# Performance work log

Hardware: AMD Instinct MI355X
Metric: run time of the kernel (lower is better)

Reference implementation:

```python
import jax, jax.numpy as jnp
import numpy as np

B, N, H, F_IN, F_OUT = 16, 512, 8, 128, 128
NEG_SLOPE = 0.2


def setup_inputs() -> dict:
    key = jax.random.key(0)
    k_h, k_adj, k_bias, k_W, k_a = jax.random.split(key, 5)
    h = jax.random.normal(k_h, (B, N, F_IN), dtype=jnp.float32)
    # Binary adjacency (shared across batch); force self-loops so every row
    # of the masked softmax has at least one valid entry (avoids NaN rows).
    adj = jax.random.randint(k_adj, (N, N), 0, 2, dtype=jnp.int32)
    adj = adj.at[jnp.arange(N), jnp.arange(N)].set(1)
    bias_matrix = jax.random.normal(k_bias, (1, 1, N, N), dtype=jnp.float32)
    # Xavier-uniform-like init for params
    lim_W = float(np.sqrt(6.0 / (F_IN + F_OUT)))
    W = jax.random.uniform(k_W, (H, F_IN, F_OUT), minval=-lim_W, maxval=lim_W, dtype=jnp.float32)
    lim_a = float(np.sqrt(6.0 / (2 * F_OUT + 1)))
    a = jax.random.uniform(k_a, (H, 2 * F_OUT, 1), minval=-lim_a, maxval=lim_a, dtype=jnp.float32)
    return {"h": h, "adj": adj, "bias_matrix": bias_matrix, "W": W, "a": a}


def reference(h, adj, bias_matrix, W, a):
    # h: [B,N,Fin], adj: [N,N] int, bias_matrix: [1,1,N,N], W: [H,Fin,F], a: [H,2F,1]
    f = W.shape[-1]
    h_prime = jnp.einsum('bni,hio->bnho', h, W)  # [B,N,H,F]
    # e[b,i,j,h] = leakyrelu(a_h . concat(h_prime[b,i,h], h_prime[b,j,h]))
    # Decompose a into src/dst halves: identical math, avoids O(B*N*N*H*2F) cat.
    a_src = a[:, :f, 0]  # [H,F]
    a_dst = a[:, f:, 0]  # [H,F]
    s_src = jnp.einsum('bnhf,hf->bnh', h_prime, a_src)  # score contribution of node i
    s_dst = jnp.einsum('bnhf,hf->bnh', h_prime, a_dst)  # score contribution of node j
    e = jax.nn.leaky_relu(s_src[:, :, None, :] + s_dst[:, None, :, :], NEG_SLOPE)  # [B,N,N,H]
    e = e + bias_matrix[0, 0][None, :, :, None]  # bias broadcast over batch & heads
    mask = (adj != 0)[None, :, :, None]  # [1,N,N,1] -> broadcast [B,N,N,H]
    e = jnp.where(mask, e, -jnp.inf)
    attention = jax.nn.softmax(e, axis=2)  # softmax over neighbors j
    h_out = jnp.einsum('bijh,bjhf->bihf', attention, h_prime)  # [B,N,H,F]
    # concat=False -> mean over heads
    return h_out.mean(axis=2)  # [B,N,F]
```

## Files before the change

### kernel.cpp

```cpp
#include <hip/hip_runtime.h>
#include <hip/hip_bf16.h>

#define NB 16
#define NN 512
#define NH 8
#define NF 128
#define NEG_SLOPE 0.2f

typedef short bf16x8 __attribute__((ext_vector_type(8)));
typedef unsigned short u16x8 __attribute__((ext_vector_type(8)));
typedef float f32x4 __attribute__((ext_vector_type(4)));

__device__ inline unsigned short f2bf(float x) {
    __hip_bfloat16 b = __float2bfloat16(x);
    return __builtin_bit_cast(unsigned short, b);
}
__device__ inline float bf2f(unsigned short u) {
    return __uint_as_float(((unsigned int)u) << 16);
}

__global__ __launch_bounds__(256) void prep_all_kernel(
    const float* __restrict__ h, const int* __restrict__ adj,
    const float* __restrict__ bias, const float* __restrict__ W,
    const float* __restrict__ a,
    float* __restrict__ mb,
    unsigned short* __restrict__ hHi, unsigned short* __restrict__ hLo,
    unsigned short* __restrict__ wtHi, unsigned short* __restrict__ wtLo,
    float* __restrict__ wasrc, float* __restrict__ wadst)
{
    int t = blockIdx.x * 256 + threadIdx.x;
    {
        float v = h[t];
        unsigned short hi = f2bf(v);
        hHi[t] = hi;
        hLo[t] = f2bf(v - bf2f(hi));
    }
    if (t < NN * NN) mb[t] = (adj[t] != 0) ? bias[t] : -1.0e30f;
    if (t < NH * NF * NF) {
        float v = W[t];
        int hh = t >> 14;
        int k  = (t >> 7) & 127;
        int f  = t & 127;
        int u  = (hh * NF + f) * NF + k;
        unsigned short hi = f2bf(v);
        wtHi[u] = hi;
        wtLo[u] = f2bf(v - bf2f(hi));
    }
    if (t < NH * NF) {
        int hh = t >> 7, i = t & 127;
        const float* wrow = W + (hh * NF + i) * NF;
        const float* asr = a + hh * 2 * NF;
        const float* ads = asr + NF;
        float s1 = 0.f, s2 = 0.f;
        #pragma unroll 4
        for (int f = 0; f < NF; ++f) {
            float w = wrow[f];
            s1 = fmaf(w, asr[f], s1);
            s2 = fmaf(w, ads[f], s2);
        }
        wasrc[t] = s1; wadst[t] = s2;
    }
}

__global__ __launch_bounds__(256) void score_kernel(
    const float* __restrict__ h, const float* __restrict__ wasrc,
    const float* __restrict__ wadst, float* __restrict__ ssrc, float* __restrict__ sdstT)
{
    __shared__ float wsm[2][NH * (NF + 4)];
    int tid = threadIdx.x;
    for (int u = tid; u < NH * NF; u += 256) {
        int hh = u >> 7, f = u & 127;
        wsm[0][hh * (NF + 4) + f] = wasrc[u];
        wsm[1][hh * (NF + 4) + f] = wadst[u];
    }
    __syncthreads();
    int t = blockIdx.x * 256 + tid;
    int hh = t & 7;
    int bn = t >> 3;
    int b = bn >> 9, n = bn & 511;
    const float4* hrow = (const float4*)(h + (size_t)bn * NF);
    const float4* w1 = (const float4*)(&wsm[0][hh * (NF + 4)]);
    const float4* w2 = (const float4*)(&wsm[1][hh * (NF + 4)]);
    float s1 = 0.f, s2 = 0.f;
    #pragma unroll
    for (int u = 0; u < NF / 4; ++u) {
        float4 hv = hrow[u], a1 = w1[u], a2 = w2[u];
        s1 += hv.x * a1.x + hv.y * a1.y + hv.z * a1.z + hv.w * a1.w;
        s2 += hv.x * a2.x + hv.y * a2.y + hv.z * a2.z + hv.w * a2.w;
    }
    ssrc[t] = s1;
    sdstT[((size_t)(b * NH + hh)) * NN + n] = s2;
}

__global__ __launch_bounds__(256, 4) void hprime_kernel(
    const unsigned short* __restrict__ hHi, const unsigned short* __restrict__ hLo,
    const unsigned short* __restrict__ wtHi, const unsigned short* __restrict__ wtLo,
    unsigned short* __restrict__ hpT)
{
    int bx = blockIdx.x;
    int nchunk = bx & 63;
    int hfg = bx >> 6;
    int hh = hfg >> 1, fg = hfg & 1;
    int tid = threadIdx.x;
    int wave = tid >> 6, lane = tid & 63;
    int col = lane & 15, kg = lane >> 4;
    int fbase = hh * NF + fg * 64 + wave * 16;
    int n0g = nchunk * 128;
    int b = n0g >> 9;
    int nin = n0g & 511;

    const unsigned short* Bh = wtHi + (size_t)(fbase + col) * NF + kg * 8;
    const unsigned short* Bl = wtLo + (size_t)(fbase + col) * NF + kg * 8;
    bf16x8 bh[4], bl[4];
    #pragma unroll
    for (int ks = 0; ks < 4; ++ks) {
        bh[ks] = *(const bf16x8*)(Bh + ks * 32);
        bl[ks] = *(const bf16x8*)(Bl + ks * 32);
    }

    size_t outRow = ((size_t)b * (NH * NF) + fbase + col) * NN;

    #pragma unroll 2
    for (int nt = 0; nt < 8; ++nt) {
        const unsigned short* Ah = hHi + (size_t)(n0g + nt * 16 + col) * NF + kg * 8;
        const unsigned short* Al = hLo + (size_t)(n0g + nt * 16 + col) * NF + kg * 8;
        bf16x8 ah[4], al[4];
        #pragma unroll
        for (int ks = 0; ks < 4; ++ks) {
            ah[ks] = *(const bf16x8*)(Ah + ks * 32);
            al[ks] = *(const bf16x8*)(Al + ks * 32);
        }
        f32x4 acc = {0.f, 0.f, 0.f, 0.f};
        #pragma unroll
        for (int ks = 0; ks < 4; ++ks) {
            acc = __builtin_amdgcn_mfma_f32_16x16x32_bf16(ah[ks], bh[ks], acc, 0, 0, 0);
            acc = __builtin_amdgcn_mfma_f32_16x16x32_bf16(al[ks], bh[ks], acc, 0, 0, 0);
            acc = __builtin_amdgcn_mfma_f32_16x16x32_bf16(ah[ks], bl[ks], acc, 0, 0, 0);
        }
        ushort4 u;
        u.x = f2bf(acc[0]); u.y = f2bf(acc[1]);
        u.z = f2bf(acc[2]); u.w = f2bf(acc[3]);
        *(ushort4*)&hpT[outRow + nin + nt * 16 + kg * 4] = u;
    }
}

__global__ __launch_bounds__(512, 4) void attn_kernel(
    const unsigned short* __restrict__ hpT, const float* __restrict__ mb,
    const float* __restrict__ ssrc, const float* __restrict__ sdstT,
    float* __restrict__ out)
{
    __shared__ float red[NH][32][64];
    int bx = blockIdx.x;
    int b = bx & 15;
    int rest = bx >> 4;
    int ipair = rest >> 1;
    int fhalf = rest & 1;
    int i0 = ipair * 32;
    int f0 = fhalf * 64;
    int tid = threadIdx.x;
    int lane = tid & 63, h = tid >> 6;
    int col = lane & 15, kg = lane >> 4;

    const short one_bf = (short)0x3f80;
    const bf16x8 vone = {one_bf, one_bf, one_bf, one_bf, one_bf, one_bf, one_bf, one_bf};

    const float* sd = sdstT + (size_t)(b * NH + h) * NN;
    float s0 = ssrc[((size_t)(b * NN) + i0 + col) * NH + h];
    float s1 = ssrc[((size_t)(b * NN) + i0 + 16 + col) * NH + h];
    const float* mb0 = mb + (size_t)(i0 + col) * NN;
    const float* mb1 = mb + (size_t)(i0 + 16 + col) * NN;
    const unsigned short* Bbase = hpT + ((size_t)(b * NH + h) * NF + f0 + col) * NN;

    f32x4 acc[2][4];
    f32x4 accS[2];
    #pragma unroll
    for (int ti = 0; ti < 2; ++ti) {
        accS[ti] = (f32x4){0.f, 0.f, 0.f, 0.f};
        #pragma unroll
        for (int tf = 0; tf < 4; ++tf) acc[ti][tf] = (f32x4){0.f, 0.f, 0.f, 0.f};
    }

    for (int t = 0; t < 16; ++t) {
        int j0 = t * 32 + kg * 8;
        float4 sv0 = *(const float4*)(sd + j0);
        float4 sv1 = *(const float4*)(sd + j0 + 4);
        float4 m00 = *(const float4*)(mb0 + j0);
        float4 m01 = *(const float4*)(mb0 + j0 + 4);
        float4 m10 = *(const float4*)(mb1 + j0);
        float4 m11 = *(const float4*)(mb1 + j0 + 4);
        bf16x8 Bv0 = *(const bf16x8*)(Bbase + (size_t)0 * 16 * NN + j0);
        bf16x8 Bv1 = *(const bf16x8*)(Bbase + (size_t)1 * 16 * NN + j0);
        bf16x8 Bv2 = *(const bf16x8*)(Bbase + (size_t)2 * 16 * NN + j0);
        bf16x8 Bv3 = *(const bf16x8*)(Bbase + (size_t)3 * 16 * NN + j0);

        u16x8 a0, a1;
        {
            float x;
            x = s0 + sv0.x; x = x > 0.f ? x : NEG_SLOPE * x; a0[0] = f2bf(__expf(x + m00.x));
            x = s0 + sv0.y; x = x > 0.f ? x : NEG_SLOPE * x; a0[1] = f2bf(__expf(x + m00.y));
            x = s0 + sv0.z; x = x > 0.f ? x : NEG_SLOPE * x; a0[2] = f2bf(__expf(x + m00.z));
            x = s0 + sv0.w; x = x > 0.f ? x : NEG_SLOPE * x; a0[3] = f2bf(__expf(x + m00.w));
            x = s0 + sv1.x; x = x > 0.f ? x : NEG_SLOPE * x; a0[4] = f2bf(__expf(x + m01.x));
            x = s0 + sv1.y; x = x > 0.f ? x : NEG_SLOPE * x; a0[5] = f2bf(__expf(x + m01.y));
            x = s0 + sv1.z; x = x > 0.f ? x : NEG_SLOPE * x; a0[6] = f2bf(__expf(x + m01.z));
            x = s0 + sv1.w; x = x > 0.f ? x : NEG_SLOPE * x; a0[7] = f2bf(__expf(x + m01.w));
            x = s1 + sv0.x; x = x > 0.f ? x : NEG_SLOPE * x; a1[0] = f2bf(__expf(x + m10.x));
            x = s1 + sv0.y; x = x > 0.f ? x : NEG_SLOPE * x; a1[1] = f2bf(__expf(x + m10.y));
            x = s1 + sv0.z; x = x > 0.f ? x : NEG_SLOPE * x; a1[2] = f2bf(__expf(x + m10.z));
            x = s1 + sv0.w; x = x > 0.f ? x : NEG_SLOPE * x; a1[3] = f2bf(__expf(x + m10.w));
            x = s1 + sv1.x; x = x > 0.f ? x : NEG_SLOPE * x; a1[4] = f2bf(__expf(x + m11.x));
            x = s1 + sv1.y; x = x > 0.f ? x : NEG_SLOPE * x; a1[5] = f2bf(__expf(x + m11.y));
            x = s1 + sv1.z; x = x > 0.f ? x : NEG_SLOPE * x; a1[6] = f2bf(__expf(x + m11.z));
            x = s1 + sv1.w; x = x > 0.f ? x : NEG_SLOPE * x; a1[7] = f2bf(__expf(x + m11.w));
        }
        bf16x8 A0 = __builtin_bit_cast(bf16x8, a0);
        bf16x8 A1 = __builtin_bit_cast(bf16x8, a1);

        __builtin_amdgcn_s_setprio(1);
        acc[0][0] = __builtin_amdgcn_mfma_f32_16x16x32_bf16(A0, Bv0, acc[0][0], 0, 0, 0);
        acc[0][1] = __builtin_amdgcn_mfma_f32_16x16x32_bf16(A0, Bv1, acc[0][1], 0, 0, 0);
        acc[0][2] = __builtin_amdgcn_mfma_f32_16x16x32_bf16(A0, Bv2, acc[0][2], 0, 0, 0);
        acc[0][3] = __builtin_amdgcn_mfma_f32_16x16x32_bf16(A0, Bv3, acc[0][3], 0, 0, 0);
        accS[0]   = __builtin_amdgcn_mfma_f32_16x16x32_bf16(A0, vone, accS[0], 0, 0, 0);
        acc[1][0] = __builtin_amdgcn_mfma_f32_16x16x32_bf16(A1, Bv0, acc[1][0], 0, 0, 0);
        acc[1][1] = __builtin_amdgcn_mfma_f32_16x16x32_bf16(A1, Bv1, acc[1][1], 0, 0, 0);
        acc[1][2] = __builtin_amdgcn_mfma_f32_16x16x32_bf16(A1, Bv2, acc[1][2], 0, 0, 0);
        acc[1][3] = __builtin_amdgcn_mfma_f32_16x16x32_bf16(A1, Bv3, acc[1][3], 0, 0, 0);
        accS[1]   = __builtin_amdgcn_mfma_f32_16x16x32_bf16(A1, vone, accS[1], 0, 0, 0);
        __builtin_amdgcn_s_setprio(0);
    }

    #pragma unroll
    for (int ti = 0; ti < 2; ++ti)
        #pragma unroll
        for (int tf = 0; tf < 4; ++tf)
            #pragma unroll
            for (int r = 0; r < 4; ++r)
                red[h][ti * 16 + kg * 4 + r][tf * 16 + col] = acc[ti][tf][r] / accS[ti][r];
    __syncthreads();

    int i = tid >> 4;
    int fq = (tid & 15) * 4;
    float4 s = {0.f, 0.f, 0.f, 0.f};
    #pragma unroll
    for (int w = 0; w < NH; ++w) {
        float4 v = *(const float4*)&red[w][i][fq];
        s.x += v.x; s.y += v.y; s.z += v.z; s.w += v.w;
    }
    s.x *= 0.125f; s.y *= 0.125f; s.z *= 0.125f; s.w *= 0.125f;
    *(float4*)&out[((size_t)(b * NN) + i0 + i) * NF + f0 + fq] = s;
}

extern "C" void kernel_launch(void* const* d_in, const int* in_sizes, int n_in,
                              void* d_out, int out_size, void* d_ws, size_t ws_size,
                              hipStream_t stream)
{
    const float* h    = (const float*)d_in[0];
    const int*   adj  = (const int*)d_in[1];
    const float* bias = (const float*)d_in[2];
    const float* W    = (const float*)d_in[3];
    const float* a    = (const float*)d_in[4];
    float* out = (float*)d_out;

    char* ws = (char*)d_ws;
    unsigned short* hpT  = (unsigned short*)ws;   ws += (size_t)NB * NH * NF * NN * 2;
    float* mb    = (float*)ws;                    ws += (size_t)NN * NN * 4;
    float* ssrc  = (float*)ws;                    ws += (size_t)NB * NN * NH * 4;
    float* sdstT = (float*)ws;                    ws += (size_t)NB * NN * NH * 4;
    float* wasrc = (float*)ws;                    ws += NH * NF * 4;
    float* wadst = (float*)ws;                    ws += NH * NF * 4;
    unsigned short* hHi  = (unsigned short*)ws;   ws += (size_t)NB * NN * NF * 2;
    unsigned short* hLo  = (unsigned short*)ws;   ws += (size_t)NB * NN * NF * 2;
    unsigned short* wtHi = (unsigned short*)ws;   ws += (size_t)NH * NF * NF * 2;
    unsigned short* wtLo = (unsigned short*)ws;   ws += (size_t)NH * NF * NF * 2;

    hipLaunchKernelGGL(prep_all_kernel, dim3((NB * NN * NF) / 256), dim3(256), 0, stream,
                       h, adj, bias, W, a, mb, hHi, hLo, wtHi, wtLo, wasrc, wadst);
    hipLaunchKernelGGL(score_kernel, dim3((NB * NN * NH) / 256), dim3(256), 0, stream,
                       h, wasrc, wadst, ssrc, sdstT);
    hipLaunchKernelGGL(hprime_kernel, dim3(64 * 16), dim3(256), 0, stream,
                       hHi, hLo, wtHi, wtLo, hpT);
    hipLaunchKernelGGL(attn_kernel, dim3(NB * 32), dim3(512), 0, stream,
                       hpT, mb, ssrc, sdstT, out);
}
```

Baseline: 181.8 us.

## Precompute exp(bias) masked bf16 and widen attention tile to full feature width

The prep kernel now stores exp(bias) as bf16, with zero where there is no edge, in place of an fp32 additive mask. This halves mask traffic, and the exponent no longer has to absorb the bias. The attention kernel now covers all 128 features per block instead of 64. That halves the grid to 256 blocks and computes the softmax numerators once rather than twice per feature half. It also software-pipelines the score and mask loads, and does the head reduction in two passes to fit a smaller shared buffer. The trade-offs are more accumulator registers (launch bounds drop to 2 blocks per CU) and fewer blocks than the GPU has compute units.

```diff
diff --git a/kernel.cpp b/kernel.cpp
--- a/kernel.cpp
+++ b/kernel.cpp
@@ -23,7 +23,7 @@
     const float* __restrict__ h, const int* __restrict__ adj,
     const float* __restrict__ bias, const float* __restrict__ W,
     const float* __restrict__ a,
-    float* __restrict__ mb,
+    unsigned short* __restrict__ emb,
     unsigned short* __restrict__ hHi, unsigned short* __restrict__ hLo,
     unsigned short* __restrict__ wtHi, unsigned short* __restrict__ wtLo,
     float* __restrict__ wasrc, float* __restrict__ wadst)
@@ -35,7 +35,7 @@
         hHi[t] = hi;
         hLo[t] = f2bf(v - bf2f(hi));
     }
-    if (t < NN * NN) mb[t] = (adj[t] != 0) ? bias[t] : -1.0e30f;
+    if (t < NN * NN) emb[t] = (adj[t] != 0) ? f2bf(__expf(bias[t])) : (unsigned short)0;
     if (t < NH * NF * NF) {
         float v = W[t];
         int hh = t >> 14;
@@ -48,15 +48,15 @@
     }
     if (t < NH * NF) {
         int hh = t >> 7, i = t & 127;
-        const float* wrow = W + (hh * NF + i) * NF;
-        const float* asr = a + hh * 2 * NF;
-        const float* ads = asr + NF;
+        const float4* wrow = (const float4*)(W + (hh * NF + i) * NF);
+        const float4* asr = (const float4*)(a + hh * 2 * NF);
+        const float4* ads = (const float4*)(a + hh * 2 * NF + NF);
         float s1 = 0.f, s2 = 0.f;
-        #pragma unroll 4
-        for (int f = 0; f < NF; ++f) {
-            float w = wrow[f];
-            s1 = fmaf(w, asr[f], s1);
-            s2 = fmaf(w, ads[f], s2);
+        #pragma unroll 8
+        for (int f = 0; f < NF / 4; ++f) {
+            float4 w = wrow[f], x = asr[f], y = ads[f];
+            s1 += w.x * x.x + w.y * x.y + w.z * x.z + w.w * x.w;
+            s2 += w.x * y.x + w.y * y.y + w.z * y.z + w.w * y.w;
         }
         wasrc[t] = s1; wadst[t] = s2;
     }
@@ -144,19 +144,31 @@
     }
 }
 
-__global__ __launch_bounds__(512, 4) void attn_kernel(
-    const unsigned short* __restrict__ hpT, const float* __restrict__ mb,
+__device__ inline bf16x8 make_afrag(float s, float4 v0, float4 v1, bf16x8 eb) {
+    u16x8 ebu = __builtin_bit_cast(u16x8, eb);
+    u16x8 r;
+    float x;
+    x = s + v0.x; x = fmaxf(x, NEG_SLOPE * x); r[0] = f2bf(__expf(x) * bf2f(ebu[0]));
+    x = s + v0.y; x = fmaxf(x, NEG_SLOPE * x); r[1] = f2bf(__expf(x) * bf2f(ebu[1]));
+    x = s + v0.z; x = fmaxf(x, NEG_SLOPE * x); r[2] = f2bf(__expf(x) * bf2f(ebu[2]));
+    x = s + v0.w; x = fmaxf(x, NEG_SLOPE * x); r[3] = f2bf(__expf(x) * bf2f(ebu[3]));
+    x = s + v1.x; x = fmaxf(x, NEG_SLOPE * x); r[4] = f2bf(__expf(x) * bf2f(ebu[4]));
+    x = s + v1.y; x = fmaxf(x, NEG_SLOPE * x); r[5] = f2bf(__expf(x) * bf2f(ebu[5]));
+    x = s + v1.z; x = fmaxf(x, NEG_SLOPE * x); r[6] = f2bf(__expf(x) * bf2f(ebu[6]));
+    x = s + v1.w; x = fmaxf(x, NEG_SLOPE * x); r[7] = f2bf(__expf(x) * bf2f(ebu[7]));
+    return __builtin_bit_cast(bf16x8, r);
+}
+
+__global__ __launch_bounds__(512, 2) void attn_kernel(
+    const unsigned short* __restrict__ hpT, const unsigned short* __restrict__ emb,
     const float* __restrict__ ssrc, const float* __restrict__ sdstT,
     float* __restrict__ out)
 {
-    __shared__ float red[NH][32][64];
+    __shared__ float red[NH][16][NF + 4];
     int bx = blockIdx.x;
     int b = bx & 15;
-    int rest = bx >> 4;
-    int ipair = rest >> 1;
-    int fhalf = rest & 1;
+    int ipair = bx >> 4;
     int i0 = ipair * 32;
-    int f0 = fhalf * 64;
     int tid = threadIdx.x;
     int lane = tid & 63, h = tid >> 6;
     int col = lane & 15, kg = lane >> 4;
@@ -167,88 +179,79 @@
     const float* sd = sdstT + (size_t)(b * NH + h) * NN;
     float s0 = ssrc[((size_t)(b * NN) + i0 + col) * NH + h];
     float s1 = ssrc[((size_t)(b * NN) + i0 + 16 + col) * NH + h];
-    const float* mb0 = mb + (size_t)(i0 + col) * NN;
-    const float* mb1 = mb + (size_t)(i0 + 16 + col) * NN;
-    const unsigned short* Bbase = hpT + ((size_t)(b * NH + h) * NF + f0 + col) * NN;
-
-    f32x4 acc[2][4];
+    const unsigned short* eb0p = emb + (size_t)(i0 + col) * NN;
+    const unsigned short* eb1p = emb + (size_t)(i0 + 16 + col) * NN;
+    const unsigned short* Bbase = hpT + ((size_t)(b * NH + h) * NF + col) * NN;
+
+    f32x4 acc[2][8];
     f32x4 accS[2];
     #pragma unroll
     for (int ti = 0; ti < 2; ++ti) {
         accS[ti] = (f32x4){0.f, 0.f, 0.f, 0.f};
         #pragma unroll
-        for (int tf = 0; tf < 4; ++tf) acc[ti][tf] = (f32x4){0.f, 0.f, 0.f, 0.f};
-    }
-
+        for (int tf = 0; tf < 8; ++tf) acc[ti][tf] = (f32x4){0.f, 0.f, 0.f, 0.f};
+    }
+
+    float4 sv0[2], sv1[2];
+    bf16x8 eb0v[2], eb1v[2];
+    {
+        int j = kg * 8;
+        sv0[0] = *(const float4*)(sd + j);
+        sv1[0] = *(const float4*)(sd + j + 4);
+        eb0v[0] = *(const bf16x8*)(eb0p + j);
+        eb1v[0] = *(const bf16x8*)(eb1p + j);
+    }
+
+    #pragma unroll
     for (int t = 0; t < 16; ++t) {
-        int j0 = t * 32 + kg * 8;
-        float4 sv0 = *(const float4*)(sd + j0);
-        float4 sv1 = *(const float4*)(sd + j0 + 4);
-        float4 m00 = *(const float4*)(mb0 + j0);
-        float4 m01 = *(const float4*)(mb0 + j0 + 4);
-        float4 m10 = *(const float4*)(mb1 + j0);
-        float4 m11 = *(const float4*)(mb1 + j0 + 4);
-        bf16x8 Bv0 = *(const bf16x8*)(Bbase + (size_t)0 * 16 * NN + j0);
-        bf16x8 Bv1 = *(const bf16x8*)(Bbase + (size_t)1 * 16 * NN + j0);
-        bf16x8 Bv2 = *(const bf16x8*)(Bbase + (size_t)2 * 16 * NN + j0);
-        bf16x8 Bv3 = *(const bf16x8*)(Bbase + (size_t)3 * 16 * NN + j0);
-
-        u16x8 a0, a1;
-        {
-            float x;
-            x = s0 + sv0.x; x = x > 0.f ? x : NEG_SLOPE * x; a0[0] = f2bf(__expf(x + m00.x));
-            x = s0 + sv0.y; x = x > 0.f ? x : NEG_SLOPE * x; a0[1] = f2bf(__expf(x + m00.y));
-            x = s0 + sv0.z; x = x > 0.f ? x : NEG_SLOPE * x; a0[2] = f2bf(__expf(x + m00.z));
-            x = s0 + sv0.w; x = x > 0.f ? x : NEG_SLOPE * x; a0[3] = f2bf(__expf(x + m00.w));
-            x = s0 + sv1.x; x = x > 0.f ? x : NEG_SLOPE * x; a0[4] = f2bf(__expf(x + m01.x));
-            x = s0 + sv1.y; x = x > 0.f ? x : NEG_SLOPE * x; a0[5] = f2bf(__expf(x + m01.y));
-            x = s0 + sv1.z; x = x > 0.f ? x : NEG_SLOPE * x; a0[6] = f2bf(__expf(x + m01.z));
-            x = s0 + sv1.w; x = x > 0.f ? x : NEG_SLOPE * x; a0[7] = f2bf(__expf(x + m01.w));
-            x = s1 + sv0.x; x = x > 0.f ? x : NEG_SLOPE * x; a1[0] = f2bf(__expf(x + m10.x));
-            x = s1 + sv0.y; x = x > 0.f ? x : NEG_SLOPE * x; a1[1] = f2bf(__expf(x + m10.y));
-            x = s1 + sv0.z; x = x > 0.f ? x : NEG_SLOPE * x; a1[2] = f2bf(__expf(x + m10.z));
-            x = s1 + sv0.w; x = x > 0.f ? x : NEG_SLOPE * x; a1[3] = f2bf(__expf(x + m10.w));
-            x = s1 + sv1.x; x = x > 0.f ? x : NEG_SLOPE * x; a1[4] = f2bf(__expf(x + m11.x));
-            x = s1 + sv1.y; x = x > 0.f ? x : NEG_SLOPE * x; a1[5] = f2bf(__expf(x + m11.y));
-            x = s1 + sv1.z; x = x > 0.f ? x : NEG_SLOPE * x; a1[6] = f2bf(__expf(x + m11.z));
-            x = s1 + sv1.w; x = x > 0.f ? x : NEG_SLOPE * x; a1[7] = f2bf(__expf(x + m11.w));
-        }
-        bf16x8 A0 = __builtin_bit_cast(bf16x8, a0);
-        bf16x8 A1 = __builtin_bit_cast(bf16x8, a1);
+        const int cur = t & 1, nxt = cur ^ 1;
+        const int jc = t * 32 + kg * 8;
+        if (t < 15) {
+            const int jn = jc + 32;
+            sv0[nxt] = *(const float4*)(sd + jn);
+            sv1[nxt] = *(const float4*)(sd + jn + 4);
+            eb0v[nxt] = *(const bf16x8*)(eb0p + jn);
+            eb1v[nxt] = *(const bf16x8*)(eb1p + jn);
+        }
+        bf16x8 Bv[8];
+        #pragma unroll
+        for (int tf = 0; tf < 8; ++tf)
+            Bv[tf] = *(const bf16x8*)(Bbase + (size_t)tf * 16 * NN + jc);
+
+        bf16x8 A0 = make_afrag(s0, sv0[cur], sv1[cur], eb0v[cur]);
+        bf16x8 A1 = make_afrag(s1, sv0[cur], sv1[cur], eb1v[cur]);
 
         __builtin_amdgcn_s_setprio(1);
-        acc[0][0] = __builtin_amdgcn_mfma_f32_16x16x32_bf16(A0, Bv0, acc[0][0], 0, 0, 0);
-        acc[0][1] = __builtin_amdgcn_mfma_f32_16x16x32_bf16(A0, Bv1, acc[0][1], 0, 0, 0);
-        acc[0][2] = __builtin_amdgcn_mfma_f32_16x16x32_bf16(A0, Bv2, acc[0][2], 0, 0, 0);
-        acc[0][3] = __builtin_amdgcn_mfma_f32_16x16x32_bf16(A0, Bv3, acc[0][3], 0, 0, 0);
-        accS[0]   = __builtin_amdgcn_mfma_f32_16x16x32_bf16(A0, vone, accS[0], 0, 0, 0);
-        acc[1][0] = __builtin_amdgcn_mfma_f32_16x16x32_bf16(A1, Bv0, acc[1][0], 0, 0, 0);
-        acc[1][1] = __builtin_amdgcn_mfma_f32_16x16x32_bf16(A1, Bv1, acc[1][1], 0, 0, 0);
-        acc[1][2] = __builtin_amdgcn_mfma_f32_16x16x32_bf16(A1, Bv2, acc[1][2], 0, 0, 0);
-        acc[1][3] = __builtin_amdgcn_mfma_f32_16x16x32_bf16(A1, Bv3, acc[1][3], 0, 0, 0);
-        accS[1]   = __builtin_amdgcn_mfma_f32_16x16x32_bf16(A1, vone, accS[1], 0, 0, 0);
+        #pragma unroll
+        for (int tf = 0; tf < 8; ++tf) {
+            acc[0][tf] = __builtin_amdgcn_mfma_f32_16x16x32_bf16(A0, Bv[tf], acc[0][tf], 0, 0, 0);
+            acc[1][tf] = __builtin_amdgcn_mfma_f32_16x16x32_bf16(A1, Bv[tf], acc[1][tf], 0, 0, 0);
+        }
+        accS[0] = __builtin_amdgcn_mfma_f32_16x16x32_bf16(A0, vone, accS[0], 0, 0, 0);
+        accS[1] = __builtin_amdgcn_mfma_f32_16x16x32_bf16(A1, vone, accS[1], 0, 0, 0);
         __builtin_amdgcn_s_setprio(0);
     }
 
-    #pragma unroll
-    for (int ti = 0; ti < 2; ++ti)
-        #pragma unroll
-        for (int tf = 0; tf < 4; ++tf)
+    int fr = tid & 127;
+    int iq = tid >> 7;
+    #pragma unroll
+    for (int ti = 0; ti < 2; ++ti) {
+        #pragma unroll
+        for (int tf = 0; tf < 8; ++tf)
             #pragma unroll
             for (int r = 0; r < 4; ++r)
-                red[h][ti * 16 + kg * 4 + r][tf * 16 + col] = acc[ti][tf][r] / accS[ti][r];
-    __syncthreads();
-
-    int i = tid >> 4;
-    int fq = (tid & 15) * 4;
-    float4 s = {0.f, 0.f, 0.f, 0.f};
-    #pragma unroll
-    for (int w = 0; w < NH; ++w) {
-        float4 v = *(const float4*)&red[w][i][fq];
-        s.x += v.x; s.y += v.y; s.z += v.z; s.w += v.w;
-    }
-    s.x *= 0.125f; s.y *= 0.125f; s.z *= 0.125f; s.w *= 0.125f;
-    *(float4*)&out[((size_t)(b * NN) + i0 + i) * NF + f0 + fq] = s;
+                red[h][kg * 4 + r][tf * 16 + col] = acc[ti][tf][r] / accS[ti][r];
+        __syncthreads();
+        #pragma unroll
+        for (int q = 0; q < 4; ++q) {
+            int i = iq * 4 + q;
+            float sacc = 0.f;
+            #pragma unroll
+            for (int w = 0; w < NH; ++w) sacc += red[w][i][fr];
+            out[((size_t)(b * NN) + i0 + ti * 16 + i) * NF + fr] = sacc * 0.125f;
+        }
+        if (ti == 0) __syncthreads();
+    }
 }
 
 extern "C" void kernel_launch(void* const* d_in, const int* in_sizes, int n_in,
@@ -264,7 +267,7 @@
 
     char* ws = (char*)d_ws;
     unsigned short* hpT  = (unsigned short*)ws;   ws += (size_t)NB * NH * NF * NN * 2;
-    float* mb    = (float*)ws;                    ws += (size_t)NN * NN * 4;
+    unsigned short* emb  = (unsigned short*)ws;   ws += (size_t)NN * NN * 2;
     float* ssrc  = (float*)ws;                    ws += (size_t)NB * NN * NH * 4;
     float* sdstT = (float*)ws;                    ws += (size_t)NB * NN * NH * 4;
     float* wasrc = (float*)ws;                    ws += NH * NF * 4;
@@ -275,11 +278,11 @@
     unsigned short* wtLo = (unsigned short*)ws;   ws += (size_t)NH * NF * NF * 2;
 
     hipLaunchKernelGGL(prep_all_kernel, dim3((NB * NN * NF) / 256), dim3(256), 0, stream,
-                       h, adj, bias, W, a, mb, hHi, hLo, wtHi, wtLo, wasrc, wadst);
+                       h, adj, bias, W, a, emb, hHi, hLo, wtHi, wtLo, wasrc, wadst);
     hipLaunchKernelGGL(score_kernel, dim3((NB * NN * NH) / 256), dim3(256), 0, stream,
                        h, wasrc, wadst, ssrc, sdstT);
     hipLaunchKernelGGL(hprime_kernel, dim3(64 * 16), dim3(256), 0, stream,
                        hHi, hLo, wtHi, wtLo, hpT);
-    hipLaunchKernelGGL(attn_kernel, dim3(NB * 32), dim3(512), 0, stream,
-                       hpT, mb, ssrc, sdstT, out);
-}
+    hipLaunchKernelGGL(attn_kernel, dim3(NB * 16), dim3(512), 0, stream,
+                       hpT, emb, ssrc, sdstT, out);
+}
```

Result: faster. 161.2 us (-11.3%).
